# Optimization experiments

Hardware: AMD Instinct MI355X
Metric: run time of the kernel (lower is better)

Reference implementation:

```python
import jax, jax.numpy as jnp
import numpy as np

N = 50000      # nodes
E = 1600000    # edges (avg degree 32)
D_IN = 32
D_EF = 16
D_H = 64
D_MSG = 32
D_UP = 32


def setup_inputs() -> dict:
    key = jax.random.key(0)
    ks = jax.random.split(key, 10)
    s = 0.05
    return {
        "x": jax.random.normal(ks[0], (N, D_IN), dtype=jnp.float32),
        "degrees": jax.random.uniform(ks[1], (N, 1), dtype=jnp.float32),
        "edge_features": jax.random.normal(ks[2], (E, D_EF), dtype=jnp.float32),
        "W1m": jax.random.normal(ks[3], (2 * D_IN + D_EF, D_H), dtype=jnp.float32) * s,
        "b1m": jnp.zeros((D_H,), dtype=jnp.float32),
        "W2m": jax.random.normal(ks[4], (D_H, D_MSG), dtype=jnp.float32) * s,
        "b2m": jnp.zeros((D_MSG,), dtype=jnp.float32),
        "W1u": jax.random.normal(ks[5], (D_IN + D_MSG, D_H), dtype=jnp.float32) * s,
        "b1u": jnp.zeros((D_H,), dtype=jnp.float32),
        "W2u": jax.random.normal(ks[6], (D_H, D_UP), dtype=jnp.float32) * s,
        "b2u": jnp.zeros((D_UP,), dtype=jnp.float32),
        "edge_index": jax.random.randint(ks[7], (2, E), 0, N, dtype=jnp.int64),
    }


def mlp2(h, W1, b1, W2, b2):
    return jax.nn.relu(h @ W1 + b1) @ W2 + b2


def reference(x, degrees, edge_features, W1m, b1m, W2m, b2m, W1u, b1u, W2u, b2u, edge_index):
    # flow = 'source_to_target': select=1 -> i = targets = edge_index[1],
    # j = sources = edge_index[0]; sparse.sum over dim 0 aggregates per target.
    src = edge_index[0]
    dst = edge_index[1]
    x_i = x[dst]                                  # [E, D_IN] target features
    x_j = x[src]                                  # [E, D_IN] source features
    msg_in = jnp.concatenate([x_i, x_j, edge_features], axis=-1)  # [E, 2*D_IN+D_EF]
    msgs = mlp2(msg_in, W1m, b1m, W2m, b2m)       # [E, D_MSG]
    agg = jax.ops.segment_sum(msgs, dst, num_segments=x.shape[0])  # [N, D_MSG]
    upd_in = jnp.concatenate([x, agg], axis=-1)   # [N, D_IN+D_MSG]
    return mlp2(upd_in, W1u, b1u, W2u, b2u)       # [N, D_UP]
```

## Files before the change

kernel.cpp:

```cpp
#include <hip/hip_runtime.h>
#include <hip/hip_bf16.h>

#define D_IN  32
#define D_EF  16
#define D_H   64
#define D_MSG 32
#define D_UP  32

typedef __fp16 v2h __attribute__((ext_vector_type(2)));

__device__ __forceinline__ unsigned bf16pair(float a, float b) {
    unsigned ua = __float_as_uint(a);
    ua = (ua + 0x7fffu + ((ua >> 16) & 1u)) >> 16;
    unsigned ub = __float_as_uint(b);
    ub = (ub + 0x7fffu + ((ub >> 16) & 1u)) >> 16;
    return ua | (ub << 16);
}
__device__ __forceinline__ float bf_lo(unsigned u) { return __uint_as_float(u << 16); }
__device__ __forceinline__ float bf_hi(unsigned u) { return __uint_as_float(u & 0xffff0000u); }

__global__ __launch_bounds__(256) void prep_kernel(
    const float* __restrict__ x,
    const float* __restrict__ W1m,
    const float* __restrict__ b1m,
    const float* __restrict__ W2m,
    const int*   __restrict__ ei,
    float* __restrict__ P1,
    unsigned short* __restrict__ P2b,
    int* __restrict__ deg,
    int* __restrict__ rank,
    v2h* __restrict__ W1Ep,
    v2h* __restrict__ W2p,
    int n_nodes, int n_edges, int NBn, int NBe)
{
    int b = blockIdx.x;

    if (b < NBn) {
        int i = b * 256 + threadIdx.x;
        if (i >= n_nodes) return;

        float xi[D_IN];
        const float4* xp = (const float4*)(x + (size_t)i * D_IN);
#pragma unroll
        for (int k4 = 0; k4 < D_IN / 4; ++k4) {
            float4 v = xp[k4];
            xi[4 * k4 + 0] = v.x; xi[4 * k4 + 1] = v.y;
            xi[4 * k4 + 2] = v.z; xi[4 * k4 + 3] = v.w;
        }
        {
            float acc[D_H];
#pragma unroll
            for (int j = 0; j < D_H; ++j) acc[j] = b1m[j];
            for (int k = 0; k < D_IN; ++k) {
                float xv = xi[k];
                const float* wr = W1m + (size_t)k * D_H;
#pragma unroll
                for (int j = 0; j < D_H; ++j) acc[j] += xv * wr[j];
            }
            float4* o = (float4*)(P1 + (size_t)i * D_H);
#pragma unroll
            for (int j4 = 0; j4 < D_H / 4; ++j4)
                o[j4] = make_float4(acc[4 * j4], acc[4 * j4 + 1],
                                    acc[4 * j4 + 2], acc[4 * j4 + 3]);
        }
        {
            float acc[D_H];
#pragma unroll
            for (int j = 0; j < D_H; ++j) acc[j] = 0.0f;
            for (int k = 0; k < D_IN; ++k) {
                float xv = xi[k];
                const float* wr = W1m + (size_t)(k + D_IN) * D_H;
#pragma unroll
                for (int j = 0; j < D_H; ++j) acc[j] += xv * wr[j];
            }
            uint4* o = (uint4*)(P2b + (size_t)i * D_H);
#pragma unroll
            for (int j8 = 0; j8 < D_H / 8; ++j8) {
                uint4 q;
                q.x = bf16pair(acc[8 * j8 + 0], acc[8 * j8 + 1]);
                q.y = bf16pair(acc[8 * j8 + 2], acc[8 * j8 + 3]);
                q.z = bf16pair(acc[8 * j8 + 4], acc[8 * j8 + 5]);
                q.w = bf16pair(acc[8 * j8 + 6], acc[8 * j8 + 7]);
                o[j8] = q;
            }
        }
    } else if (b < NBn + NBe) {
        int e = (b - NBn) * 256 + threadIdx.x;
        if (e < n_edges)
            rank[e] = atomicAdd(&deg[ei[n_edges + e]], 1);
    } else {
        int t = threadIdx.x;
        const float* W1E = W1m + (size_t)(2 * D_IN) * D_H;
        for (int idx = t; idx < 8 * D_H; idx += 256) {
            int kp = idx >> 6, c = idx & 63;
            W1Ep[idx] = __builtin_amdgcn_cvt_pkrtz(W1E[(2 * kp) * D_H + c],
                                                   W1E[(2 * kp + 1) * D_H + c]);
        }
        for (int idx = t; idx < 32 * D_MSG; idx += 256) {
            int jp = idx >> 5, m = idx & 31;
            W2p[idx] = __builtin_amdgcn_cvt_pkrtz(W2m[(2 * jp) * D_MSG + m],
                                                  W2m[(2 * jp + 1) * D_MSG + m]);
        }
    }
}

__global__ __launch_bounds__(256) void scan_partials_kernel(
    const int* __restrict__ deg, int* __restrict__ bsum, int n_nodes)
{
    int idx = blockIdx.x * 256 + threadIdx.x;
    int v = (idx < n_nodes) ? deg[idx] : 0;
#pragma unroll
    for (int o = 1; o < 64; o <<= 1) v += __shfl_xor(v, o, 64);
    __shared__ int ws[4];
    int lane = threadIdx.x & 63, w = threadIdx.x >> 6;
    if (lane == 0) ws[w] = v;
    __syncthreads();
    if (threadIdx.x == 0) bsum[blockIdx.x] = ws[0] + ws[1] + ws[2] + ws[3];
}

__global__ __launch_bounds__(256) void scan_blockoffs_kernel(
    const int* __restrict__ bsum, int* __restrict__ boffs, int nb)
{
    __shared__ int sdata[256];
    int t = threadIdx.x;
    sdata[t] = (t < nb) ? bsum[t] : 0;
    __syncthreads();
    for (int off = 1; off < 256; off <<= 1) {
        int u = (t >= off) ? sdata[t - off] : 0;
        __syncthreads();
        sdata[t] += u;
        __syncthreads();
    }
    if (t < nb) boffs[t] = (t > 0) ? sdata[t - 1] : 0;
}

__global__ __launch_bounds__(256) void scan_final_kernel(
    const int* __restrict__ deg, const int* __restrict__ boffs,
    int* __restrict__ offs, int n_nodes)
{
    __shared__ int sdata[256];
    int t = threadIdx.x;
    int idx = blockIdx.x * 256 + t;
    sdata[t] = (idx < n_nodes) ? deg[idx] : 0;
    __syncthreads();
    for (int off = 1; off < 256; off <<= 1) {
        int u = (t >= off) ? sdata[t - off] : 0;
        __syncthreads();
        sdata[t] += u;
        __syncthreads();
    }
    int excl = boffs[blockIdx.x] + ((t > 0) ? sdata[t - 1] : 0);
    if (idx < n_nodes) offs[idx] = excl;
}

__global__ __launch_bounds__(256) void scatter_kernel(
    const int* __restrict__ ei,
    const int* __restrict__ rank,
    const int* __restrict__ offs,
    int2* __restrict__ edges_sorted,
    int n_edges)
{
    int e = blockIdx.x * blockDim.x + threadIdx.x;
    if (e < n_edges) {
        int s = ei[e];
        int d = ei[n_edges + e];
        int pos = offs[d] + rank[e];
        edges_sorted[pos] = make_int2(e, s);
    }
}

__global__ __launch_bounds__(256) void gather_kernel(
    const float* __restrict__ ef,
    const v2h*  __restrict__ W1Ep,
    const v2h*  __restrict__ W2p,
    const float* __restrict__ P1,
    const unsigned short* __restrict__ P2b,
    const int*  __restrict__ deg,
    const int*  __restrict__ offs,
    const int2* __restrict__ edges_sorted,
    float* __restrict__ agg,
    int n_nodes)
{
    int tid = blockIdx.x * blockDim.x + threadIdx.x;
    int n = tid >> 4;
    int t = tid & 15;
    if (n >= n_nodes) return;

    int start = offs[n];
    int end   = start + deg[n];
    const float* P1n = P1 + (size_t)n * D_H;

    float msg[D_MSG];
#pragma unroll
    for (int m = 0; m < D_MSG; ++m) msg[m] = 0.0f;

    int i = start + t;
    int s = 0;
    float4 ef0, ef1, ef2, ef3;
    if (i < end) {
        int2 es = edges_sorted[i];
        s = es.y;
        const float4* efp = (const float4*)(ef + (size_t)es.x * D_EF);
        ef0 = efp[0]; ef1 = efp[1]; ef2 = efp[2]; ef3 = efp[3];
    }

    while (i < end) {
        int inext = i + 16;
        int ip = (inext < end) ? inext : i;
        int2 es2 = edges_sorted[ip];
        const float4* efp2 = (const float4*)(ef + (size_t)es2.x * D_EF);
        float4 nf0 = efp2[0], nf1 = efp2[1], nf2 = efp2[2], nf3 = efp2[3];

        v2h efh[D_EF / 2];
        efh[0] = __builtin_amdgcn_cvt_pkrtz(ef0.x, ef0.y);
        efh[1] = __builtin_amdgcn_cvt_pkrtz(ef0.z, ef0.w);
        efh[2] = __builtin_amdgcn_cvt_pkrtz(ef1.x, ef1.y);
        efh[3] = __builtin_amdgcn_cvt_pkrtz(ef1.z, ef1.w);
        efh[4] = __builtin_amdgcn_cvt_pkrtz(ef2.x, ef2.y);
        efh[5] = __builtin_amdgcn_cvt_pkrtz(ef2.z, ef2.w);
        efh[6] = __builtin_amdgcn_cvt_pkrtz(ef3.x, ef3.y);
        efh[7] = __builtin_amdgcn_cvt_pkrtz(ef3.z, ef3.w);

        const float4* p1  = (const float4*)P1n;
        const uint4*  p2u = (const uint4*)(P2b + (size_t)s * D_H);
        uint4 b = p2u[0];

#pragma unroll 1
        for (int j = 0; j < D_H / 8; ++j) {
            int jn = (j < D_H / 8 - 1) ? (j + 1) : 0;
            uint4 c = p2u[jn];

            float4 a0 = p1[2 * j], a1 = p1[2 * j + 1];
            float h[8];
            h[0] = a0.x + bf_lo(b.x); h[1] = a0.y + bf_hi(b.x);
            h[2] = a0.z + bf_lo(b.y); h[3] = a0.w + bf_hi(b.y);
            h[4] = a1.x + bf_lo(b.z); h[5] = a1.y + bf_hi(b.z);
            h[6] = a1.z + bf_lo(b.w); h[7] = a1.w + bf_hi(b.w);

#pragma unroll
            for (int kp = 0; kp < D_EF / 2; ++kp) {
                const v2h* wr = W1Ep + kp * D_H + 8 * j;
#pragma unroll
                for (int c8 = 0; c8 < 8; ++c8)
                    h[c8] = __builtin_amdgcn_fdot2(efh[kp], wr[c8], h[c8], false);
            }

            v2h hp[4];
#pragma unroll
            for (int cp = 0; cp < 4; ++cp) {
                float r0 = h[2 * cp]     > 0.0f ? h[2 * cp]     : 0.0f;
                float r1 = h[2 * cp + 1] > 0.0f ? h[2 * cp + 1] : 0.0f;
                hp[cp] = __builtin_amdgcn_cvt_pkrtz(r0, r1);
            }

#pragma unroll
            for (int cp = 0; cp < 4; ++cp) {
                const v2h* wr2 = W2p + (size_t)(4 * j + cp) * D_MSG;
#pragma unroll
                for (int m = 0; m < D_MSG; ++m)
                    msg[m] = __builtin_amdgcn_fdot2(hp[cp], wr2[m], msg[m], false);
            }
            b = c;
        }

        i = inext; s = es2.y;
        ef0 = nf0; ef1 = nf1; ef2 = nf2; ef3 = nf3;
    }

#pragma unroll
    for (int m = 0; m < D_MSG; ++m) {
        float v = msg[m];
        v += __shfl_xor(v, 1, 16);
        v += __shfl_xor(v, 2, 16);
        v += __shfl_xor(v, 4, 16);
        v += __shfl_xor(v, 8, 16);
        msg[m] = v;
    }

    if (t == 0) {
        float4* ap = (float4*)(agg + (size_t)n * D_MSG);
#pragma unroll
        for (int m4 = 0; m4 < D_MSG / 4; ++m4)
            ap[m4] = make_float4(msg[4 * m4], msg[4 * m4 + 1],
                                 msg[4 * m4 + 2], msg[4 * m4 + 3]);
    }
}

__global__ __launch_bounds__(256) void node_upd_kernel(
    const float* __restrict__ x,
    const float* __restrict__ agg,
    const int*   __restrict__ deg,
    const float* __restrict__ b2m,
    const float* __restrict__ W1u,
    const float* __restrict__ b1u,
    const float* __restrict__ W2u,
    const float* __restrict__ b2u,
    float* __restrict__ out,
    int n_nodes)
{
    int i = blockIdx.x * blockDim.x + threadIdx.x;
    if (i >= n_nodes) return;

    float in[D_IN + D_MSG];
    const float4* xp = (const float4*)(x + (size_t)i * D_IN);
#pragma unroll
    for (int k4 = 0; k4 < D_IN / 4; ++k4) {
        float4 v = xp[k4];
        in[4 * k4 + 0] = v.x; in[4 * k4 + 1] = v.y;
        in[4 * k4 + 2] = v.z; in[4 * k4 + 3] = v.w;
    }
    float dc = (float)deg[i];
    const float4* ap = (const float4*)(agg + (size_t)i * D_MSG);
#pragma unroll
    for (int k4 = 0; k4 < D_MSG / 4; ++k4) {
        float4 v = ap[k4];
        in[D_IN + 4 * k4 + 0] = v.x + dc * b2m[4 * k4 + 0];
        in[D_IN + 4 * k4 + 1] = v.y + dc * b2m[4 * k4 + 1];
        in[D_IN + 4 * k4 + 2] = v.z + dc * b2m[4 * k4 + 2];
        in[D_IN + 4 * k4 + 3] = v.w + dc * b2m[4 * k4 + 3];
    }

    float h[D_H];
#pragma unroll
    for (int j = 0; j < D_H; ++j) h[j] = b1u[j];
    for (int k = 0; k < D_IN + D_MSG; ++k) {
        float v = in[k];
        const float* wr = W1u + (size_t)k * D_H;
#pragma unroll
        for (int j = 0; j < D_H; ++j) h[j] += v * wr[j];
    }

    float o[D_UP];
#pragma unroll
    for (int m = 0; m < D_UP; ++m) o[m] = b2u[m];
    for (int j = 0; j < D_H; ++j) {
        float r = h[j] > 0.0f ? h[j] : 0.0f;
        const float* wr = W2u + (size_t)j * D_UP;
#pragma unroll
        for (int m = 0; m < D_UP; ++m) o[m] += r * wr[m];
    }

    float4* op = (float4*)(out + (size_t)i * D_UP);
#pragma unroll
    for (int m4 = 0; m4 < D_UP / 4; ++m4)
        op[m4] = make_float4(o[4 * m4], o[4 * m4 + 1], o[4 * m4 + 2], o[4 * m4 + 3]);
}

extern "C" void kernel_launch(void* const* d_in, const int* in_sizes, int n_in,
                              void* d_out, int out_size, void* d_ws, size_t ws_size,
                              hipStream_t stream) {
    const float* x    = (const float*)d_in[0];
    const float* ef   = (const float*)d_in[2];
    const float* W1m  = (const float*)d_in[3];
    const float* b1m  = (const float*)d_in[4];
    const float* W2m  = (const float*)d_in[5];
    const float* b2m  = (const float*)d_in[6];
    const float* W1u  = (const float*)d_in[7];
    const float* b1u  = (const float*)d_in[8];
    const float* W2u  = (const float*)d_in[9];
    const float* b2u  = (const float*)d_in[10];
    const int*   ei   = (const int*)d_in[11];

    const int n_nodes = in_sizes[0] / D_IN;
    const int n_edges = in_sizes[11] / 2;

    float* out = (float*)d_out;

    const int NBn = (n_nodes + 255) / 256;
    const int NBe = (n_edges + 255) / 256;

    float*          agg = (float*)d_ws;
    float*          P1  = agg + (size_t)n_nodes * D_MSG;
    unsigned short* P2b = (unsigned short*)(P1 + (size_t)n_nodes * D_H);
    int2* edges_sorted  = (int2*)(P2b + (size_t)n_nodes * D_H);
    int* rank   = (int*)(edges_sorted + n_edges);
    int* deg    = rank   + n_edges;
    int* offs   = deg    + n_nodes;
    int* bsum   = offs   + n_nodes;
    int* boffs  = bsum   + NBn;
    v2h* W1Ep   = (v2h*)(boffs + NBn);
    v2h* W2p    = W1Ep + 8 * D_H;

    hipMemsetAsync(deg, 0, (size_t)n_nodes * sizeof(int), stream);

    prep_kernel<<<NBn + NBe + 1, 256, 0, stream>>>(
        x, W1m, b1m, W2m, ei, P1, P2b, deg, rank, W1Ep, W2p,
        n_nodes, n_edges, NBn, NBe);

    scan_partials_kernel<<<NBn, 256, 0, stream>>>(deg, bsum, n_nodes);
    scan_blockoffs_kernel<<<1, 256, 0, stream>>>(bsum, boffs, NBn);
    scan_final_kernel<<<NBn, 256, 0, stream>>>(deg, boffs, offs, n_nodes);

    scatter_kernel<<<NBe, 256, 0, stream>>>(ei, rank, offs, edges_sorted, n_edges);

    {
        long total = (long)n_nodes * 16;
        int grid = (int)((total + 255) / 256);
        gather_kernel<<<grid, 256, 0, stream>>>(ef, W1Ep, W2p, P1, P2b,
                                                deg, offs, edges_sorted, agg,
                                                n_nodes);
    }
    node_upd_kernel<<<NBn, 256, 0, stream>>>(x, agg, deg, b2m,
                                             W1u, b1u, W2u, b2u, out, n_nodes);
}
```

Before: 485.9 us.

## Sum ReLU hidden activations per node and apply W2m after aggregation

Because the second message layer is linear, the per-edge W2m matmul is moved after the segment sum. The gather kernel now accumulates the 64-wide ReLU hidden vector per target node and reduces it across the 16 lanes with a transposing shuffle tree, writing a 64-float row per node. The node update kernel then applies W2m once per node. This removes 64x32 fdot2 work per edge in exchange for more accumulator registers and a larger per-node intermediate buffer, which now aliases the rank buffer.

```diff
diff --git a/kernel.cpp b/kernel.cpp
--- a/kernel.cpp
+++ b/kernel.cpp
@@ -23,14 +23,12 @@
     const float* __restrict__ x,
     const float* __restrict__ W1m,
     const float* __restrict__ b1m,
-    const float* __restrict__ W2m,
     const int*   __restrict__ ei,
     float* __restrict__ P1,
     unsigned short* __restrict__ P2b,
     int* __restrict__ deg,
     int* __restrict__ rank,
     v2h* __restrict__ W1Ep,
-    v2h* __restrict__ W2p,
     int n_nodes, int n_edges, int NBn, int NBe)
 {
     int b = blockIdx.x;
@@ -96,11 +94,6 @@
             W1Ep[idx] = __builtin_amdgcn_cvt_pkrtz(W1E[(2 * kp) * D_H + c],
                                                    W1E[(2 * kp + 1) * D_H + c]);
         }
-        for (int idx = t; idx < 32 * D_MSG; idx += 256) {
-            int jp = idx >> 5, m = idx & 31;
-            W2p[idx] = __builtin_amdgcn_cvt_pkrtz(W2m[(2 * jp) * D_MSG + m],
-                                                  W2m[(2 * jp + 1) * D_MSG + m]);
-        }
     }
 }
 
@@ -172,13 +165,12 @@
 __global__ __launch_bounds__(256) void gather_kernel(
     const float* __restrict__ ef,
     const v2h*  __restrict__ W1Ep,
-    const v2h*  __restrict__ W2p,
     const float* __restrict__ P1,
     const unsigned short* __restrict__ P2b,
     const int*  __restrict__ deg,
     const int*  __restrict__ offs,
     const int2* __restrict__ edges_sorted,
-    float* __restrict__ agg,
+    float* __restrict__ hagg,
     int n_nodes)
 {
     int tid = blockIdx.x * blockDim.x + threadIdx.x;
@@ -190,9 +182,9 @@
     int end   = start + deg[n];
     const float* P1n = P1 + (size_t)n * D_H;
 
-    float msg[D_MSG];
-#pragma unroll
-    for (int m = 0; m < D_MSG; ++m) msg[m] = 0.0f;
+    float hacc[D_H];
+#pragma unroll
+    for (int c = 0; c < D_H; ++c) hacc[c] = 0.0f;
 
     int i = start + t;
     int s = 0;
@@ -223,13 +215,10 @@
 
         const float4* p1  = (const float4*)P1n;
         const uint4*  p2u = (const uint4*)(P2b + (size_t)s * D_H);
-        uint4 b = p2u[0];
-
-#pragma unroll 1
+
+#pragma unroll
         for (int j = 0; j < D_H / 8; ++j) {
-            int jn = (j < D_H / 8 - 1) ? (j + 1) : 0;
-            uint4 c = p2u[jn];
-
+            uint4 b = p2u[j];
             float4 a0 = p1[2 * j], a1 = p1[2 * j + 1];
             float h[8];
             h[0] = a0.x + bf_lo(b.x); h[1] = a0.y + bf_hi(b.x);
@@ -245,52 +234,68 @@
                     h[c8] = __builtin_amdgcn_fdot2(efh[kp], wr[c8], h[c8], false);
             }
 
-            v2h hp[4];
-#pragma unroll
-            for (int cp = 0; cp < 4; ++cp) {
-                float r0 = h[2 * cp]     > 0.0f ? h[2 * cp]     : 0.0f;
-                float r1 = h[2 * cp + 1] > 0.0f ? h[2 * cp + 1] : 0.0f;
-                hp[cp] = __builtin_amdgcn_cvt_pkrtz(r0, r1);
+#pragma unroll
+            for (int c8 = 0; c8 < 8; ++c8) {
+                float r = h[c8] > 0.0f ? h[c8] : 0.0f;
+                hacc[8 * j + c8] += r;
             }
-
-#pragma unroll
-            for (int cp = 0; cp < 4; ++cp) {
-                const v2h* wr2 = W2p + (size_t)(4 * j + cp) * D_MSG;
-#pragma unroll
-                for (int m = 0; m < D_MSG; ++m)
-                    msg[m] = __builtin_amdgcn_fdot2(hp[cp], wr2[m], msg[m], false);
-            }
-            b = c;
         }
 
         i = inext; s = es2.y;
         ef0 = nf0; ef1 = nf1; ef2 = nf2; ef3 = nf3;
     }
 
-#pragma unroll
-    for (int m = 0; m < D_MSG; ++m) {
-        float v = msg[m];
-        v += __shfl_xor(v, 1, 16);
-        v += __shfl_xor(v, 2, 16);
-        v += __shfl_xor(v, 4, 16);
-        v += __shfl_xor(v, 8, 16);
-        msg[m] = v;
-    }
-
-    if (t == 0) {
-        float4* ap = (float4*)(agg + (size_t)n * D_MSG);
-#pragma unroll
-        for (int m4 = 0; m4 < D_MSG / 4; ++m4)
-            ap[m4] = make_float4(msg[4 * m4], msg[4 * m4 + 1],
-                                 msg[4 * m4 + 2], msg[4 * m4 + 3]);
-    }
+    float r1[32];
+    {
+        const bool up = (t & 8) != 0;
+#pragma unroll
+        for (int c = 0; c < 32; ++c) {
+            float lo = hacc[c]      + __shfl_xor(hacc[c],      8, 16);
+            float hi = hacc[c + 32] + __shfl_xor(hacc[c + 32], 8, 16);
+            r1[c] = up ? hi : lo;
+        }
+    }
+    float r2[16];
+    {
+        const bool up = (t & 4) != 0;
+#pragma unroll
+        for (int c = 0; c < 16; ++c) {
+            float lo = r1[c]      + __shfl_xor(r1[c],      4, 16);
+            float hi = r1[c + 16] + __shfl_xor(r1[c + 16], 4, 16);
+            r2[c] = up ? hi : lo;
+        }
+    }
+    float r3[8];
+    {
+        const bool up = (t & 2) != 0;
+#pragma unroll
+        for (int c = 0; c < 8; ++c) {
+            float lo = r2[c]     + __shfl_xor(r2[c],     2, 16);
+            float hi = r2[c + 8] + __shfl_xor(r2[c + 8], 2, 16);
+            r3[c] = up ? hi : lo;
+        }
+    }
+    float r4[4];
+    {
+        const bool up = (t & 1) != 0;
+#pragma unroll
+        for (int c = 0; c < 4; ++c) {
+            float lo = r3[c]     + __shfl_xor(r3[c],     1, 16);
+            float hi = r3[c + 4] + __shfl_xor(r3[c + 4], 1, 16);
+            r4[c] = up ? hi : lo;
+        }
+    }
+
+    ((float4*)(hagg + (size_t)n * D_H))[t] =
+        make_float4(r4[0], r4[1], r4[2], r4[3]);
 }
 
 __global__ __launch_bounds__(256) void node_upd_kernel(
     const float* __restrict__ x,
-    const float* __restrict__ agg,
+    const float* __restrict__ hagg,
     const int*   __restrict__ deg,
     const float* __restrict__ b2m,
+    const float* __restrict__ W2m,
     const float* __restrict__ W1u,
     const float* __restrict__ b1u,
     const float* __restrict__ W2u,
@@ -309,15 +314,21 @@
         in[4 * k4 + 0] = v.x; in[4 * k4 + 1] = v.y;
         in[4 * k4 + 2] = v.z; in[4 * k4 + 3] = v.w;
     }
+
     float dc = (float)deg[i];
-    const float4* ap = (const float4*)(agg + (size_t)i * D_MSG);
-#pragma unroll
-    for (int k4 = 0; k4 < D_MSG / 4; ++k4) {
-        float4 v = ap[k4];
-        in[D_IN + 4 * k4 + 0] = v.x + dc * b2m[4 * k4 + 0];
-        in[D_IN + 4 * k4 + 1] = v.y + dc * b2m[4 * k4 + 1];
-        in[D_IN + 4 * k4 + 2] = v.z + dc * b2m[4 * k4 + 2];
-        in[D_IN + 4 * k4 + 3] = v.w + dc * b2m[4 * k4 + 3];
+#pragma unroll
+    for (int m = 0; m < D_MSG; ++m) in[D_IN + m] = dc * b2m[m];
+
+    const float4* hp = (const float4*)(hagg + (size_t)i * D_H);
+    for (int j4 = 0; j4 < D_H / 4; ++j4) {
+        float4 v = hp[j4];
+        const float* w0 = W2m + (size_t)(4 * j4 + 0) * D_MSG;
+        const float* w1 = W2m + (size_t)(4 * j4 + 1) * D_MSG;
+        const float* w2 = W2m + (size_t)(4 * j4 + 2) * D_MSG;
+        const float* w3 = W2m + (size_t)(4 * j4 + 3) * D_MSG;
+#pragma unroll
+        for (int m = 0; m < D_MSG; ++m)
+            in[D_IN + m] += v.x * w0[m] + v.y * w1[m] + v.z * w2[m] + v.w * w3[m];
     }
 
     float h[D_H];
@@ -369,22 +380,21 @@
     const int NBn = (n_nodes + 255) / 256;
     const int NBe = (n_edges + 255) / 256;
 
-    float*          agg = (float*)d_ws;
-    float*          P1  = agg + (size_t)n_nodes * D_MSG;
+    float*          P1  = (float*)d_ws;
     unsigned short* P2b = (unsigned short*)(P1 + (size_t)n_nodes * D_H);
     int2* edges_sorted  = (int2*)(P2b + (size_t)n_nodes * D_H);
-    int* rank   = (int*)(edges_sorted + n_edges);
-    int* deg    = rank   + n_edges;
+    int* deg    = (int*)(edges_sorted + n_edges);
     int* offs   = deg    + n_nodes;
     int* bsum   = offs   + n_nodes;
     int* boffs  = bsum   + NBn;
     v2h* W1Ep   = (v2h*)(boffs + NBn);
-    v2h* W2p    = W1Ep + 8 * D_H;
+    int*   rank = (int*)(W1Ep + 8 * D_H);
+    float* hagg = (float*)rank;
 
     hipMemsetAsync(deg, 0, (size_t)n_nodes * sizeof(int), stream);
 
     prep_kernel<<<NBn + NBe + 1, 256, 0, stream>>>(
-        x, W1m, b1m, W2m, ei, P1, P2b, deg, rank, W1Ep, W2p,
+        x, W1m, b1m, ei, P1, P2b, deg, rank, W1Ep,
         n_nodes, n_edges, NBn, NBe);
 
     scan_partials_kernel<<<NBn, 256, 0, stream>>>(deg, bsum, n_nodes);
@@ -396,10 +406,10 @@
     {
         long total = (long)n_nodes * 16;
         int grid = (int)((total + 255) / 256);
-        gather_kernel<<<grid, 256, 0, stream>>>(ef, W1Ep, W2p, P1, P2b,
-                                                deg, offs, edges_sorted, agg,
+        gather_kernel<<<grid, 256, 0, stream>>>(ef, W1Ep, P1, P2b,
+                                                deg, offs, edges_sorted, hagg,
                                                 n_nodes);
     }
-    node_upd_kernel<<<NBn, 256, 0, stream>>>(x, agg, deg, b2m,
+    node_upd_kernel<<<NBn, 256, 0, stream>>>(x, hagg, deg, b2m, W2m,
                                              W1u, b1u, W2u, b2u, out, n_nodes);
 }
```

Result: slower. 516.5 us (+6.3%).
